# Performance work log

Measured on AMD Instinct MI355X. Metric: run time of the kernel, lower is better.

The kernel has to match this reference:

```python
import jax, jax.numpy as jnp
import numpy as np

DIM = 64
HEADS = 8
K_RATIOS = [0.5, 0.67, 0.75, 0.8]
BN_EPS = 1e-5


def conv3d(x, w, b, groups=1, pad=0):
    out = jax.lax.conv_general_dilated(
        x, w, window_strides=(1, 1, 1), padding=[(pad, pad)] * 3,
        dimension_numbers=('NCDHW', 'OIDHW', 'NCDHW'),
        feature_group_count=groups)
    return out + b[None, :, None, None, None]


def bn_eval(x, gamma, beta):
    # BatchNorm3d in inference mode with init running stats (mean=0, var=1)
    s = gamma / np.float32(np.sqrt(1.0 + BN_EPS))
    return x * s[None, :, None, None, None] + beta[None, :, None, None, None]


def setup_inputs() -> dict:
    key = jax.random.key(0)
    ks = jax.random.split(key, 12)
    def p(k, shape, scale=0.05):
        return jax.random.normal(k, shape, dtype=jnp.float32) * scale
    B, D, H, W = 2, 16, 64, 64
    return {
        'x': jax.random.normal(ks[0], (B, DIM, D, H, W), dtype=jnp.float32),
        'w_qkv': p(ks[1], (3 * DIM, DIM, 1, 1, 1)),
        'b_qkv': p(ks[2], (3 * DIM,)),
        'w_dw': p(ks[3], (3 * DIM, 1, 3, 3, 3)),
        'b_dw': p(ks[4], (3 * DIM,)),
        'temperature': jnp.ones((HEADS, 1, 1), jnp.float32),
        'attn_weights': jnp.ones((len(K_RATIOS),), jnp.float32),
        'w_recal': p(ks[5], (DIM, DIM, 1, 1, 1)),
        'b_recal': p(ks[6], (DIM,)),
        'bn1_g': jnp.ones((DIM,), jnp.float32),
        'bn1_b': jnp.zeros((DIM,), jnp.float32),
        'w_fus': p(ks[7], (DIM, 2 * DIM, 1, 1, 1)),
        'b_fus': p(ks[8], (DIM,)),
        'bn2_g': jnp.ones((DIM,), jnp.float32),
        'bn2_b': jnp.zeros((DIM,), jnp.float32),
        'w_proj': p(ks[9], (DIM, DIM, 1, 1, 1)),
        'b_proj': p(ks[10], (DIM,)),
    }


def reference(x, w_qkv, b_qkv, w_dw, b_dw, temperature, attn_weights,
              w_recal, b_recal, bn1_g, bn1_b, w_fus, b_fus, bn2_g, bn2_b,
              w_proj, b_proj):
    b, c, d, h, w = x.shape
    residual = x
    qkv = conv3d(conv3d(x, w_qkv, b_qkv), w_dw, b_dw, groups=3 * DIM, pad=1)
    q, k, v = jnp.split(qkv, 3, axis=1)
    def to_heads(t):  # b (head ch) d h w -> b head ch (d h w)
        return t.reshape(b, HEADS, c // HEADS, d * h * w)
    q, k, v = to_heads(q), to_heads(k), to_heads(v)
    # L2-normalize along token dim (torch F.normalize, eps=1e-12)
    q = q / jnp.maximum(jnp.linalg.norm(q, axis=-1, keepdims=True), 1e-12)
    k = k / jnp.maximum(jnp.linalg.norm(k, axis=-1, keepdims=True), 1e-12)
    C = q.shape[2]
    attn = jnp.einsum('bhin,bhjn->bhij', q, k) * temperature[None]  # (b,head,C,C)
    soft_w = jax.nn.softmax(attn_weights)
    weighted = 0.0
    for i, ratio in enumerate(K_RATIOS):
        kv = int(C * ratio)
        idx = jax.lax.top_k(attn, kv)[1]                      # (b,head,C,kv)
        mask = jax.nn.one_hot(idx, C, dtype=attn.dtype).sum(-2) > 0
        probs = jax.nn.softmax(jnp.where(mask, attn, -jnp.inf), axis=-1)
        out = jnp.einsum('bhij,bhjn->bhin', probs, v)          # (b,head,C,N)
        weighted = weighted + soft_w[i] * out.reshape(b, c, d, h, w)
    recalib = jax.nn.sigmoid(bn_eval(conv3d(weighted, w_recal, b_recal), bn1_g, bn1_b))
    enhanced = weighted * recalib
    fused = jnp.concatenate([enhanced, residual], axis=1)
    output = bn_eval(conv3d(fused, w_fus, b_fus), bn2_g, bn2_b)
    output = conv3d(output, w_proj, b_proj)
    return output
```

## Files before the change

### kernel.cpp

```cpp
#include <hip/hip_runtime.h>
#include <math.h>

#define NPOS 65536
#define DD 16
#define HHH 64
#define WWW 64
#define K3CHUNK 64

typedef __attribute__((ext_vector_type(8))) _Float16 h16x8;
typedef __attribute__((ext_vector_type(4))) short s16x4;
typedef __attribute__((ext_vector_type(4))) float f32x4;
typedef __attribute__((ext_vector_type(2))) _Float16 f16x2;

static __device__ __forceinline__ short f2h(float f) {
    union { _Float16 h; short s; } v; v.h = (_Float16)f; return v.s;
}
static __device__ __forceinline__ float h2f(short s) {
    union { short s; _Float16 h; } v; v.s = s; return (float)v.h;
}
static __device__ __forceinline__ f16x2 i2h(int i) {
    union { int i; f16x2 h; } v; v.i = i; return v.h;
}
static __device__ __forceinline__ int h2i(f16x2 h) {
    union { int i; f16x2 h; } v; v.h = h; return v.i;
}
static __device__ __forceinline__ float fdot2f(f16x2 a, f16x2 b, float c) {
#if __has_builtin(__builtin_amdgcn_fdot2)
    return __builtin_amdgcn_fdot2(a, b, c, false);
#else
    return fmaf((float)a[0], (float)b[0], fmaf((float)a[1], (float)b[1], c));
#endif
}

__global__ void k0_prep(const float* __restrict__ Wq,
                        const float* __restrict__ Wr, const float* __restrict__ Wf,
                        const float* __restrict__ Wp,
                        const float* __restrict__ brec,
                        const float* __restrict__ bn1g, const float* __restrict__ bn1b,
                        const float* __restrict__ bfus,
                        const float* __restrict__ bn2g, const float* __restrict__ bn2b,
                        short* __restrict__ WqA, short* __restrict__ WrA,
                        short* __restrict__ WfA, short* __restrict__ WpA,
                        float* __restrict__ bias1, float* __restrict__ bias2) {
    const float invs = 1.0f / sqrtf(1.0f + 1e-5f);
    int idx = blockIdx.x * 256 + threadIdx.x;
    if (idx < 12288) {
        int e = idx & 7, l = (idx >> 3) & 63, m = (idx >> 9) & 3;
        int t = (idx >> 11) & 1, c = idx >> 12;
        int out = c*64 + 16*m + (l & 15), k = 32*t + ((l >> 4) << 3) + e;
        WqA[idx] = f2h(Wq[out*64 + k]);
        return;
    }
    int i = idx - 12288;
    if (i < 4096) {
        int e = i & 7, l = (i >> 3) & 63, m = (i >> 9) & 3, t = (i >> 11) & 1;
        int out = 16*m + (l & 15), k = 32*t + ((l >> 4) << 3) + e;
        WrA[i] = f2h(Wr[out*64 + k] * bn1g[out] * invs);
        return;
    }
    i -= 4096;
    if (i < 8192) {
        int e = i & 7, l = (i >> 3) & 63, m = (i >> 9) & 3, t = (i >> 11) & 3;
        int out = 16*m + (l & 15), k = 32*t + ((l >> 4) << 3) + e;
        WfA[i] = f2h(Wf[out*128 + k] * bn2g[out] * invs);
        return;
    }
    i -= 8192;
    if (i < 4096) {
        int e = i & 7, l = (i >> 3) & 63, m = (i >> 9) & 3, t = (i >> 11) & 1;
        int out = 16*m + (l & 15), k = 32*t + ((l >> 4) << 3) + e;
        WpA[i] = f2h(Wp[out*64 + k]);
        return;
    }
    i -= 4096;
    if (i < 64)       bias1[i]    = brec[i]    * bn1g[i]    * invs + bn1b[i];
    else if (i < 128) bias2[i-64] = bfus[i-64] * bn2g[i-64] * invs + bn2b[i-64];
}

__global__ __launch_bounds__(256) void k1_qkv(const float* __restrict__ x,
        const short* __restrict__ WqA, const float* __restrict__ bq,
        short* __restrict__ qkv) {
    __shared__ __align__(16) float Xs[64 * 64];
    const int tid = threadIdx.x, lane = tid & 63, wv = tid >> 6;
    const int blk = blockIdx.x;
    const int b = blk >> 10, n0 = (blk & 1023) << 6;
    const float* xg = x + ((long long)b * 64) * NPOS + n0;
    #pragma unroll
    for (int kk = 0; kk < 4; ++kk) {
        int idx = tid + kk * 256;
        int ch = idx >> 4, p = (idx & 15) << 2;
        *(float4*)(Xs + ch * 64 + p) = *(const float4*)(xg + (long long)ch * NPOS + p);
    }
    const int bcol  = wv * 16 + (lane & 15);
    const int bk    = (lane >> 4) << 3;
    const int drow0 = (lane >> 4) << 2;
    __syncthreads();

    h16x8 B0, B1;
    #pragma unroll
    for (int e = 0; e < 8; ++e) B0[e] = (_Float16)Xs[(bk + e) * 64 + bcol];
    #pragma unroll
    for (int e = 0; e < 8; ++e) B1[e] = (_Float16)Xs[(32 + bk + e) * 64 + bcol];

    short* outb = qkv + ((long long)b * 192) * NPOS + n0 + bcol;
    #pragma unroll
    for (int c = 0; c < 3; ++c) {
        #pragma unroll
        for (int m = 0; m < 4; ++m) {
            h16x8 A0 = *(const h16x8*)(WqA + (((c * 2 + 0) * 4 + m) * 64 + lane) * 8);
            h16x8 A1 = *(const h16x8*)(WqA + (((c * 2 + 1) * 4 + m) * 64 + lane) * 8);
            f32x4 a = {0.f, 0.f, 0.f, 0.f};
            a = __builtin_amdgcn_mfma_f32_16x16x32_f16(A0, B0, a, 0, 0, 0);
            a = __builtin_amdgcn_mfma_f32_16x16x32_f16(A1, B1, a, 0, 0, 0);
            float4 bb = *(const float4*)(bq + c * 64 + 16 * m + drow0);
            a[0] += bb.x; a[1] += bb.y; a[2] += bb.z; a[3] += bb.w;
            #pragma unroll
            for (int r = 0; r < 4; ++r)
                outb[(long long)(c * 64 + 16 * m + drow0 + r) * NPOS] = f2h(a[r]);
        }
    }
}

__global__ __launch_bounds__(256) void k2_dw(const short* __restrict__ qkv,
        const float* __restrict__ Wd, const float* __restrict__ bd,
        short* __restrict__ qkv2) {
    __shared__ __align__(16) _Float16 tile[108 * 72];
    __shared__ unsigned wpk01[9], wpk2z[9];
    __shared__ float bsh[1];
    const int tid = threadIdx.x;
    const int lane = tid & 63;
    const int bc  = blockIdx.x >> 4;
    const int sub = blockIdx.x & 15;
    const int d0  = (sub >> 2) << 2;
    const int h0  = (sub & 3) << 4;
    const int c   = bc % 192;

    if (tid < 9) {
        const float* wb = Wd + c * 27 + tid * 3;
        f16x2 a = {(_Float16)wb[0], (_Float16)wb[1]};
        f16x2 z = {(_Float16)wb[2], (_Float16)0.f};
        wpk01[tid] = (unsigned)h2i(a);
        wpk2z[tid] = (unsigned)h2i(z);
    }
    if (tid == 31) bsh[0] = bd[c];

    const short* in = qkv + (long long)bc * NPOS;
    for (int i = tid; i < 864; i += 256) {
        const int r = i >> 3, q8 = i & 7;
        const int dd = r / 18;
        const int hh = r - dd * 18;
        const int d = d0 + dd - 1;
        const int h = h0 + hh - 1;
        int4 u = make_int4(0, 0, 0, 0);
        if (d >= 0 && d < DD && h >= 0 && h < HHH)
            u = *(const int4*)(in + (d << 12) + (h << 6) + (q8 << 3));
        *(int4*)(tile + r * 72 + (q8 << 3)) = u;
    }
    __syncthreads();

    unsigned w01r[9], w2zr[9];
    #pragma unroll
    for (int s = 0; s < 9; ++s) { w01r[s] = wpk01[s]; w2zr[s] = wpk2z[s]; }
    const float bias = bsh[0];

    const int wl = tid & 15;
    const int oh = tid >> 4;
    const int w0 = wl << 2;

    float acc[4][4];
    #pragma unroll
    for (int od = 0; od < 4; ++od)
        #pragma unroll
        for (int j = 0; j < 4; ++j) acc[od][j] = bias;

    #pragma unroll
    for (int kh = 0; kh < 3; ++kh) {
        #pragma unroll
        for (int dp = 0; dp < 6; ++dp) {
            const int2 dd2 = *(const int2*)(tile + (dp * 18 + oh + kh) * 72 + w0);
            int Ldw = __shfl(dd2.y, (lane + 63) & 63, 64);
            int Rdw = __shfl(dd2.x, (lane + 1) & 63, 64);
            Ldw = (wl == 0)  ? 0 : Ldw;
            Rdw = (wl == 15) ? 0 : Rdw;
            int pr[5];
            pr[0] = __builtin_amdgcn_alignbit(dd2.x, Ldw, 16);
            pr[1] = dd2.x;
            pr[2] = __builtin_amdgcn_alignbit(dd2.y, dd2.x, 16);
            pr[3] = dd2.y;
            pr[4] = __builtin_amdgcn_alignbit(Rdw, dd2.y, 16);
            #pragma unroll
            for (int od = 0; od < 4; ++od) {
                const int kd = dp - od;
                if (kd < 0 || kd > 2) continue;
                const f16x2 w01 = i2h((int)w01r[kd * 3 + kh]);
                const f16x2 w2z = i2h((int)w2zr[kd * 3 + kh]);
                #pragma unroll
                for (int j = 0; j < 4; ++j) {
                    acc[od][j] = fdot2f(w01, i2h(pr[j]), acc[od][j]);
                    acc[od][j] = fdot2f(w2z, i2h(pr[j + 2]), acc[od][j]);
                }
            }
        }
    }
    short* outp = qkv2 + (long long)bc * NPOS + (h0 + oh) * 64 + w0;
    #pragma unroll
    for (int od = 0; od < 4; ++od) {
        s16x4 o;
        #pragma unroll
        for (int j = 0; j < 4; ++j) o[j] = f2h(acc[od][j]);
        *(s16x4*)(outp + ((d0 + od) << 12)) = o;
    }
}

__global__ __launch_bounds__(256) void k3_gram(const short* __restrict__ qkv2,
                                               float* __restrict__ partial) {
    const int blk = blockIdx.x;
    const int chunk = blk & (K3CHUNK - 1);
    const int bh = blk >> 6;
    const int b = bh >> 3, h = bh & 7;
    const int tid = threadIdx.x, lane = tid & 63, wv = tid >> 6;
    const short* base = qkv2 + ((long long)b * 192 + h * 8) * NPOS;
    const int ch = lane & 15;
    const long long roff = (ch < 8 ? (long long)ch : (long long)(56 + ch)) * NPOS;
    const short* p = base + roff + chunk * 1024 + wv * 256 + ((lane >> 4) << 3);

    f32x4 a0 = {0.f, 0.f, 0.f, 0.f}, a1 = {0.f, 0.f, 0.f, 0.f};
    #pragma unroll
    for (int it = 0; it < 4; ++it) {
        h16x8 f0 = *(const h16x8*)(p + it * 64);
        h16x8 f1 = *(const h16x8*)(p + it * 64 + 32);
        a0 = __builtin_amdgcn_mfma_f32_16x16x32_f16(f0, f0, a0, 0, 0, 0);
        a1 = __builtin_amdgcn_mfma_f32_16x16x32_f16(f1, f1, a1, 0, 0, 0);
    }
    __shared__ float gs[4][256];
    #pragma unroll
    for (int r = 0; r < 4; ++r)
        gs[wv][(((lane >> 4) << 2) + r) * 16 + (lane & 15)] = a0[r] + a1[r];
    __syncthreads();
    const int row = tid >> 4, col = tid & 15;
    float v = gs[0][tid] + gs[1][tid] + gs[2][tid] + gs[3][tid];
    float* pp = partial + ((long long)bh * K3CHUNK + chunk) * 80;
    if (row < 8 && col >= 8)      pp[row * 8 + (col - 8)] = v;
    else if (row == col && row < 8) pp[64 + row] = v;
    else if (row == col)            pp[72 + row - 8] = v;
}

__global__ __launch_bounds__(256) void k34_combine(const float* __restrict__ partial,
        const float* __restrict__ temp, const float* __restrict__ aw,
        short* __restrict__ PA) {
    __shared__ float gram[1280];
    __shared__ float P[1024];
    const int tid = threadIdx.x;
    for (int s = tid; s < 1280; s += 256) {
        int bh = s / 80, slot = s % 80;
        float acc = 0.f;
        for (int c = 0; c < K3CHUNK; ++c)
            acc += partial[((long long)bh * K3CHUNK + c) * 80 + slot];
        gram[s] = acc;
    }
    __syncthreads();
    if (tid < 128) {
        int bh = tid >> 3, i = tid & 7;
        int h = bh & 7;
        const float* g = gram + bh * 80;
        float qn = fmaxf(sqrtf(g[64 + i]), 1e-12f);
        float tp = temp[h];
        float attn[8];
        #pragma unroll
        for (int j = 0; j < 8; ++j) {
            float kn = fmaxf(sqrtf(g[72 + j]), 1e-12f);
            attn[j] = g[i * 8 + j] / (qn * kn) * tp;
        }
        float awv[4];
        float am = -3.4e38f;
        for (int r = 0; r < 4; ++r) { awv[r] = aw[r]; am = fmaxf(am, awv[r]); }
        float asum = 0.f;
        for (int r = 0; r < 4; ++r) { awv[r] = expf(awv[r] - am); asum += awv[r]; }
        const int kvs[4] = {4, 5, 6, 6};
        float Pacc[8];
        #pragma unroll
        for (int j = 0; j < 8; ++j) Pacc[j] = 0.f;
        for (int r = 0; r < 4; ++r) {
            float sw = awv[r] / asum;
            int kv = kvs[r];
            bool sel[8];
            #pragma unroll
            for (int j = 0; j < 8; ++j) sel[j] = false;
            for (int m = 0; m < kv; ++m) {
                int best = 0; float bv = -3.4e38f;
                for (int j = 0; j < 8; ++j)
                    if (!sel[j] && attn[j] > bv) { bv = attn[j]; best = j; }
                sel[best] = true;
            }
            float mx = -3.4e38f;
            for (int j = 0; j < 8; ++j) if (sel[j]) mx = fmaxf(mx, attn[j]);
            float es = 0.f, e[8];
            for (int j = 0; j < 8; ++j) { e[j] = sel[j] ? expf(attn[j] - mx) : 0.f; es += e[j]; }
            for (int j = 0; j < 8; ++j) Pacc[j] += sw * e[j] / es;
        }
        for (int j = 0; j < 8; ++j) P[tid * 8 + j] = Pacc[j];
    }
    __syncthreads();
    for (int idx = tid; idx < 8192; idx += 256) {
        int e = idx & 7, l = (idx >> 3) & 63, m = (idx >> 9) & 3;
        int t = (idx >> 11) & 1, b = idx >> 12;
        int out = 16*m + (l & 15), k = 32*t + ((l >> 4) << 3) + e;
        float v = ((k >> 3) == (out >> 3)) ? P[(b * 64 + out) * 8 + (k & 7)] : 0.f;
        PA[idx] = f2h(v);
    }
}

__global__ __launch_bounds__(256) void k5_tail(
        const short* __restrict__ qkv2, const float* __restrict__ x,
        const short* __restrict__ PA, const short* __restrict__ WrA,
        const short* __restrict__ WfA, const short* __restrict__ WpA,
        const float* __restrict__ bias1, const float* __restrict__ bias2,
        const float* __restrict__ bp, float* __restrict__ out) {
    __shared__ __align__(16) float As[64 * 64];
    __shared__ __align__(16) float Xs[64 * 64];
    const int tid = threadIdx.x, lane = tid & 63, wv = tid >> 6;
    const int blk = blockIdx.x;
    const int b = blk >> 10, n0 = (blk & 1023) << 6;
    const short* vg = qkv2 + ((long long)b * 192 + 128) * NPOS + n0;
    const float* xg = x + ((long long)b * 64) * NPOS + n0;
    #pragma unroll
    for (int kk = 0; kk < 4; ++kk) {
        int idx = tid + kk * 256;
        int ch = idx >> 4, p = (idx & 15) << 2;
        *(float4*)(Xs + ch * 64 + p) = *(const float4*)(xg + (long long)ch * NPOS + p);
    }
    #pragma unroll
    for (int kk = 0; kk < 2; ++kk) {
        int i = tid + kk * 256;
        int ch = i >> 3, p0 = (i & 7) << 3;
        h16x8 raw = *(const h16x8*)(vg + (long long)ch * NPOS + p0);
        *(float4*)(As + ch * 64 + p0) =
            make_float4((float)raw[0], (float)raw[1], (float)raw[2], (float)raw[3]);
        *(float4*)(As + ch * 64 + p0 + 4) =
            make_float4((float)raw[4], (float)raw[5], (float)raw[6], (float)raw[7]);
    }
    h16x8 pA[2][4];
    #pragma unroll
    for (int t = 0; t < 2; ++t)
        #pragma unroll
        for (int m = 0; m < 4; ++m)
            pA[t][m] = *(const h16x8*)(PA + (((b * 2 + t) * 4 + m) * 64 + lane) * 8);
    const int bcol  = wv * 16 + (lane & 15);
    const int bk    = (lane >> 4) << 3;
    const int drow0 = (lane >> 4) << 2;
    __syncthreads();

    auto loadB = [&](const float* S, int kbase) {
        h16x8 r;
        #pragma unroll
        for (int e = 0; e < 8; ++e) r[e] = (_Float16)S[(kbase + bk + e) * 64 + bcol];
        return r;
    };

    f32x4 Dw[4];
    {
        h16x8 B0 = loadB(As, 0), B1 = loadB(As, 32);
        #pragma unroll
        for (int m = 0; m < 4; ++m) {
            f32x4 a = {0.f, 0.f, 0.f, 0.f};
            a = __builtin_amdgcn_mfma_f32_16x16x32_f16(pA[0][m], B0, a, 0, 0, 0);
            a = __builtin_amdgcn_mfma_f32_16x16x32_f16(pA[1][m], B1, a, 0, 0, 0);
            Dw[m] = a;
        }
    }
    #pragma unroll
    for (int m = 0; m < 4; ++m)
        #pragma unroll
        for (int r = 0; r < 4; ++r)
            As[(16 * m + drow0 + r) * 64 + bcol] = Dw[m][r];

    float enh[4][4];
    {
        h16x8 rA[2][4];
        #pragma unroll
        for (int t = 0; t < 2; ++t)
            #pragma unroll
            for (int m = 0; m < 4; ++m)
                rA[t][m] = *(const h16x8*)(WrA + ((t * 4 + m) * 64 + lane) * 8);
        h16x8 B0 = loadB(As, 0), B1 = loadB(As, 32);
        #pragma unroll
        for (int m = 0; m < 4; ++m) {
            f32x4 a = {0.f, 0.f, 0.f, 0.f};
            a = __builtin_amdgcn_mfma_f32_16x16x32_f16(rA[0][m], B0, a, 0, 0, 0);
            a = __builtin_amdgcn_mfma_f32_16x16x32_f16(rA[1][m], B1, a, 0, 0, 0);
            #pragma unroll
            for (int r = 0; r < 4; ++r) {
                float z = a[r] + bias1[16 * m + drow0 + r];
                enh[m][r] = Dw[m][r] / (1.f + expf(-z));
            }
        }
    }
    #pragma unroll
    for (int m = 0; m < 4; ++m)
        #pragma unroll
        for (int r = 0; r < 4; ++r)
            As[(16 * m + drow0 + r) * 64 + bcol] = enh[m][r];

    f32x4 D3[4];
    {
        h16x8 fA[4][4];
        #pragma unroll
        for (int t = 0; t < 4; ++t)
            #pragma unroll
            for (int m = 0; m < 4; ++m)
                fA[t][m] = *(const h16x8*)(WfA + ((t * 4 + m) * 64 + lane) * 8);
        h16x8 B0 = loadB(As, 0), B1 = loadB(As, 32);
        h16x8 B2 = loadB(Xs, 0), B3 = loadB(Xs, 32);
        #pragma unroll
        for (int m = 0; m < 4; ++m) {
            f32x4 a = {0.f, 0.f, 0.f, 0.f};
            a = __builtin_amdgcn_mfma_f32_16x16x32_f16(fA[0][m], B0, a, 0, 0, 0);
            a = __builtin_amdgcn_mfma_f32_16x16x32_f16(fA[1][m], B1, a, 0, 0, 0);
            a = __builtin_amdgcn_mfma_f32_16x16x32_f16(fA[2][m], B2, a, 0, 0, 0);
            a = __builtin_amdgcn_mfma_f32_16x16x32_f16(fA[3][m], B3, a, 0, 0, 0);
            #pragma unroll
            for (int r = 0; r < 4; ++r) a[r] += bias2[16 * m + drow0 + r];
            D3[m] = a;
        }
    }
    #pragma unroll
    for (int m = 0; m < 4; ++m)
        #pragma unroll
        for (int r = 0; r < 4; ++r)
            As[(16 * m + drow0 + r) * 64 + bcol] = D3[m][r];

    {
        h16x8 qA[2][4];
        #pragma unroll
        for (int t = 0; t < 2; ++t)
            #pragma unroll
            for (int m = 0; m < 4; ++m)
                qA[t][m] = *(const h16x8*)(WpA + ((t * 4 + m) * 64 + lane) * 8);
        h16x8 B0 = loadB(As, 0), B1 = loadB(As, 32);
        float* outb = out + ((long long)b * 64) * NPOS + n0 + bcol;
        #pragma unroll
        for (int m = 0; m < 4; ++m) {
            f32x4 a = {0.f, 0.f, 0.f, 0.f};
            a = __builtin_amdgcn_mfma_f32_16x16x32_f16(qA[0][m], B0, a, 0, 0, 0);
            a = __builtin_amdgcn_mfma_f32_16x16x32_f16(qA[1][m], B1, a, 0, 0, 0);
            #pragma unroll
            for (int r = 0; r < 4; ++r)
                outb[(long long)(16 * m + drow0 + r) * NPOS] =
                    a[r] + bp[16 * m + drow0 + r];
        }
    }
}

extern "C" void kernel_launch(void* const* d_in, const int* in_sizes, int n_in,
                              void* d_out, int out_size, void* d_ws, size_t ws_size,
                              hipStream_t stream) {
    (void)in_sizes; (void)n_in; (void)out_size; (void)ws_size;
    const float* x     = (const float*)d_in[0];
    const float* w_qkv = (const float*)d_in[1];
    const float* b_qkv = (const float*)d_in[2];
    const float* w_dw  = (const float*)d_in[3];
    const float* b_dw  = (const float*)d_in[4];
    const float* temp  = (const float*)d_in[5];
    const float* aw    = (const float*)d_in[6];
    const float* w_rec = (const float*)d_in[7];
    const float* b_rec = (const float*)d_in[8];
    const float* bn1g  = (const float*)d_in[9];
    const float* bn1b  = (const float*)d_in[10];
    const float* w_fus = (const float*)d_in[11];
    const float* b_fus = (const float*)d_in[12];
    const float* bn2g  = (const float*)d_in[13];
    const float* bn2b  = (const float*)d_in[14];
    const float* w_prj = (const float*)d_in[15];
    const float* b_prj = (const float*)d_in[16];
    float* out = (float*)d_out;

    short* qkv  = (short*)d_ws;
    short* qkv2 = qkv + 25165824;
    float* part = (float*)(qkv2 + 25165824);
    float* bias1 = part + 81920;
    float* bias2 = bias1 + 64;
    short* WqA  = (short*)(bias2 + 64);
    short* WrA  = WqA + 12288;
    short* WfA  = WrA + 4096;
    short* WpA  = WfA + 8192;
    short* PAb  = WpA + 4096;

    k0_prep<<<113, 256, 0, stream>>>(w_qkv, w_rec, w_fus, w_prj, b_rec, bn1g, bn1b,
                                     b_fus, bn2g, bn2b, WqA, WrA, WfA, WpA, bias1, bias2);
    k1_qkv<<<2048, 256, 0, stream>>>(x, WqA, b_qkv, qkv);
    k2_dw<<<6144, 256, 0, stream>>>(qkv, w_dw, b_dw, qkv2);
    k3_gram<<<16 * K3CHUNK, 256, 0, stream>>>(qkv2, part);
    k34_combine<<<1, 256, 0, stream>>>(part, temp, aw, PAb);
    k5_tail<<<2048, 256, 0, stream>>>(qkv2, x, PAb, WrA, WfA, WpA,
                                      bias1, bias2, b_prj, out);
}
```

Before: 110.4 us.

## Enlarge depthwise conv tile to 8 depths and 8 widths per thread

```diff
diff --git a/kernel.cpp b/kernel.cpp
--- a/kernel.cpp
+++ b/kernel.cpp
@@ -14,9 +14,6 @@
 
 static __device__ __forceinline__ short f2h(float f) {
     union { _Float16 h; short s; } v; v.h = (_Float16)f; return v.s;
-}
-static __device__ __forceinline__ float h2f(short s) {
-    union { short s; _Float16 h; } v; v.s = s; return (float)v.h;
 }
 static __device__ __forceinline__ f16x2 i2h(int i) {
     union { int i; f16x2 h; } v; v.i = i; return v.h;
@@ -124,14 +121,13 @@
 __global__ __launch_bounds__(256) void k2_dw(const short* __restrict__ qkv,
         const float* __restrict__ Wd, const float* __restrict__ bd,
         short* __restrict__ qkv2) {
-    __shared__ __align__(16) _Float16 tile[108 * 72];
+    __shared__ __align__(16) _Float16 tile[180 * 80];
     __shared__ unsigned wpk01[9], wpk2z[9];
     __shared__ float bsh[1];
     const int tid = threadIdx.x;
-    const int lane = tid & 63;
-    const int bc  = blockIdx.x >> 4;
-    const int sub = blockIdx.x & 15;
-    const int d0  = (sub >> 2) << 2;
+    const int bc  = blockIdx.x >> 3;
+    const int sub = blockIdx.x & 7;
+    const int d0  = (sub >> 2) << 3;
     const int h0  = (sub & 3) << 4;
     const int c   = bc % 192;
 
@@ -144,8 +140,12 @@
     }
     if (tid == 31) bsh[0] = bd[c];
 
+    for (int r = tid; r < 180; r += 256) {
+        *(int4*)(tile + r * 80)      = make_int4(0, 0, 0, 0);
+        *(int4*)(tile + r * 80 + 72) = make_int4(0, 0, 0, 0);
+    }
     const short* in = qkv + (long long)bc * NPOS;
-    for (int i = tid; i < 864; i += 256) {
+    for (int i = tid; i < 1440; i += 256) {
         const int r = i >> 3, q8 = i & 7;
         const int dd = r / 18;
         const int hh = r - dd * 18;
@@ -154,7 +154,7 @@
         int4 u = make_int4(0, 0, 0, 0);
         if (d >= 0 && d < DD && h >= 0 && h < HHH)
             u = *(const int4*)(in + (d << 12) + (h << 6) + (q8 << 3));
-        *(int4*)(tile + r * 72 + (q8 << 3)) = u;
+        *(int4*)(tile + r * 80 + 8 + (q8 << 3)) = u;
     }
     __syncthreads();
 
@@ -163,52 +163,57 @@
     for (int s = 0; s < 9; ++s) { w01r[s] = wpk01[s]; w2zr[s] = wpk2z[s]; }
     const float bias = bsh[0];
 
-    const int wl = tid & 15;
-    const int oh = tid >> 4;
-    const int w0 = wl << 2;
-
-    float acc[4][4];
-    #pragma unroll
-    for (int od = 0; od < 4; ++od)
-        #pragma unroll
-        for (int j = 0; j < 4; ++j) acc[od][j] = bias;
+    const int wg = tid & 7;
+    const int oh = (tid >> 3) & 15;
+    const int o0 = (tid >> 7) << 2;
+    const int w0 = wg << 3;
+
+    float acc[4][8];
+    #pragma unroll
+    for (int odr = 0; odr < 4; ++odr)
+        #pragma unroll
+        for (int j = 0; j < 8; ++j) acc[odr][j] = bias;
 
     #pragma unroll
     for (int kh = 0; kh < 3; ++kh) {
         #pragma unroll
         for (int dp = 0; dp < 6; ++dp) {
-            const int2 dd2 = *(const int2*)(tile + (dp * 18 + oh + kh) * 72 + w0);
-            int Ldw = __shfl(dd2.y, (lane + 63) & 63, 64);
-            int Rdw = __shfl(dd2.x, (lane + 1) & 63, 64);
-            Ldw = (wl == 0)  ? 0 : Ldw;
-            Rdw = (wl == 15) ? 0 : Rdw;
-            int pr[5];
-            pr[0] = __builtin_amdgcn_alignbit(dd2.x, Ldw, 16);
-            pr[1] = dd2.x;
-            pr[2] = __builtin_amdgcn_alignbit(dd2.y, dd2.x, 16);
-            pr[3] = dd2.y;
-            pr[4] = __builtin_amdgcn_alignbit(Rdw, dd2.y, 16);
-            #pragma unroll
-            for (int od = 0; od < 4; ++od) {
-                const int kd = dp - od;
+            const _Float16* row = tile + ((o0 + dp) * 18 + oh + kh) * 80;
+            const int  L  = *(const int*) (row + w0 + 6);
+            const int4 d4 = *(const int4*)(row + w0 + 8);
+            const int  R  = *(const int*) (row + w0 + 16);
+            int P[10];
+            P[0] = __builtin_amdgcn_alignbit(d4.x, L, 16);
+            P[1] = d4.x;
+            P[2] = __builtin_amdgcn_alignbit(d4.y, d4.x, 16);
+            P[3] = d4.y;
+            P[4] = __builtin_amdgcn_alignbit(d4.z, d4.y, 16);
+            P[5] = d4.z;
+            P[6] = __builtin_amdgcn_alignbit(d4.w, d4.z, 16);
+            P[7] = d4.w;
+            P[8] = __builtin_amdgcn_alignbit(R, d4.w, 16);
+            P[9] = R;
+            #pragma unroll
+            for (int odr = 0; odr < 4; ++odr) {
+                const int kd = dp - odr;
                 if (kd < 0 || kd > 2) continue;
                 const f16x2 w01 = i2h((int)w01r[kd * 3 + kh]);
                 const f16x2 w2z = i2h((int)w2zr[kd * 3 + kh]);
                 #pragma unroll
-                for (int j = 0; j < 4; ++j) {
-                    acc[od][j] = fdot2f(w01, i2h(pr[j]), acc[od][j]);
-                    acc[od][j] = fdot2f(w2z, i2h(pr[j + 2]), acc[od][j]);
+                for (int j = 0; j < 8; ++j) {
+                    acc[odr][j] = fdot2f(w01, i2h(P[j]), acc[odr][j]);
+                    acc[odr][j] = fdot2f(w2z, i2h(P[j + 2]), acc[odr][j]);
                 }
             }
         }
     }
     short* outp = qkv2 + (long long)bc * NPOS + (h0 + oh) * 64 + w0;
     #pragma unroll
-    for (int od = 0; od < 4; ++od) {
-        s16x4 o;
-        #pragma unroll
-        for (int j = 0; j < 4; ++j) o[j] = f2h(acc[od][j]);
-        *(s16x4*)(outp + ((d0 + od) << 12)) = o;
+    for (int odr = 0; odr < 4; ++odr) {
+        union { s16x4 s4[2]; int4 i4; } o;
+        #pragma unroll
+        for (int j = 0; j < 8; ++j) o.s4[j >> 2][j & 3] = f2h(acc[odr][j]);
+        *(int4*)(outp + ((d0 + o0 + odr) << 12)) = o.i4;
     }
 }
 
@@ -488,7 +493,7 @@
     k0_prep<<<113, 256, 0, stream>>>(w_qkv, w_rec, w_fus, w_prj, b_rec, bn1g, bn1b,
                                      b_fus, bn2g, bn2b, WqA, WrA, WfA, WpA, bias1, bias2);
     k1_qkv<<<2048, 256, 0, stream>>>(x, WqA, b_qkv, qkv);
-    k2_dw<<<6144, 256, 0, stream>>>(qkv, w_dw, b_dw, qkv2);
+    k2_dw<<<3072, 256, 0, stream>>>(qkv, w_dw, b_dw, qkv2);
     k3_gram<<<16 * K3CHUNK, 256, 0, stream>>>(qkv2, part);
     k34_combine<<<1, 256, 0, stream>>>(part, temp, aw, PAb);
     k5_tail<<<2048, 256, 0, stream>>>(qkv2, x, PAb, WrA, WfA, WpA,
```

New measurement: 117.0 us. +6.0%, slower.
